# Kernel tuning notes

Hardware: AMD Instinct MI355X
Metric: run time of the kernel (lower is better)

## Reference

```python
import jax, jax.numpy as jnp
import numpy as np

SCALE = 10000.0
EPS = 1e-5


def _extract_patches(x):
    # x: [B,28,28] int32 -> [B,28,28,9] (3x3 neighborhoods, zero-padded)
    xp = jnp.pad(x, ((0, 0), (1, 1), (1, 1)))
    ps = [xp[:, i:i + 28, j:j + 28] for i in range(3) for j in range(3)]
    return jnp.stack(ps, axis=-1)


def _bn_eval(x, g, b, m, v):
    inv = g / jnp.sqrt(v + EPS)
    return x * inv[None, :, None, None] + (b - m * inv)[None, :, None, None]


def _maxpool2(x):
    return jax.lax.reduce_window(x, -jnp.inf, jax.lax.max,
                                 (1, 1, 2, 2), (1, 1, 2, 2), 'VALID')


def _conv(x, w, b):
    y = jax.lax.conv_general_dilated(x, w, (1, 1), 'SAME',
                                     dimension_numbers=('NCHW', 'OIHW', 'NCHW'))
    return y + b[None, :, None, None]


def setup_inputs() -> dict:
    key = jax.random.key(0)
    ks = jax.random.split(key, 24)
    B = 1024
    inp = {}
    inp['x_img'] = jax.random.randint(ks[0], (B, 28, 28), 0, 256, dtype=jnp.int32)
    # quantized conv1 weights: round(w * 10000), signed
    inp['y_int'] = jax.random.randint(ks[1], (16, 9), 0, 20001, dtype=jnp.int32) - 10000
    inp['bias1'] = jax.random.normal(ks[2], (16,), jnp.float32)
    for i, (c, kg, kb, km, kv) in enumerate([(16, 3, 4, 5, 6), (32, 7, 8, 9, 10), (64, 11, 12, 13, 14)]):
        j = i + 1
        inp[f'g{j}'] = jax.random.uniform(ks[kg], (c,), jnp.float32, 0.5, 1.5)
        inp[f'b{j}'] = jax.random.normal(ks[kb], (c,), jnp.float32)
        inp[f'm{j}'] = jax.random.normal(ks[km], (c,), jnp.float32)
        inp[f'v{j}'] = jax.random.uniform(ks[kv], (c,), jnp.float32, 0.5, 1.5)
    inp['w2'] = jax.random.normal(ks[15], (32, 16, 3, 3), jnp.float32) * 0.1
    inp['bias2'] = jax.random.normal(ks[16], (32,), jnp.float32)
    inp['w3'] = jax.random.normal(ks[17], (64, 32, 3, 3), jnp.float32) * 0.1
    inp['bias3'] = jax.random.normal(ks[18], (64,), jnp.float32)
    inp['w_fc1'] = jax.random.normal(ks[19], (128, 576), jnp.float32) * 0.05
    inp['b_fc1'] = jax.random.normal(ks[20], (128,), jnp.float32)
    inp['w_fc2'] = jax.random.normal(ks[21], (10, 128), jnp.float32) * 0.1
    inp['b_fc2'] = jax.random.normal(ks[22], (10,), jnp.float32)
    return inp


def reference(x_img, y_int, bias1, g1, b1, m1, v1, w2, bias2, g2, b2, m2, v2,
              w3, bias3, g3, b3, m3, v3, w_fc1, b_fc1, w_fc2, b_fc2):
    # IPFE first conv: exact integer inner product <patch, y>, then /10000 + bias
    patches = _extract_patches(x_img)                      # [B,28,28,9] int32
    ip = jnp.einsum('bhwk,ok->bohw', patches, y_int)       # exact int32 dot
    feat = ip.astype(jnp.float32) / SCALE + bias1[None, :, None, None]  # [B,16,28,28]
    feat = _maxpool2(jax.nn.relu(_bn_eval(feat, g1, b1, m1, v1)))       # [B,16,14,14]
    feat = _maxpool2(jax.nn.relu(_bn_eval(_conv(feat, w2, bias2), g2, b2, m2, v2)))  # [B,32,7,7]
    feat = _maxpool2(jax.nn.relu(_bn_eval(_conv(feat, w3, bias3), g3, b3, m3, v3)))  # [B,64,3,3]
    flat = feat.reshape(feat.shape[0], -1)                 # [B,576]
    h = jax.nn.relu(flat @ w_fc1.T + b_fc1)                # [B,128] (dropout: eval mode)
    return h @ w_fc2.T + b_fc2                             # [B,10]
```

## Files before the change

kernel.cpp:

```cpp
#include <hip/hip_runtime.h>
#include <hip/hip_bf16.h>

#define EPS 1e-5f

typedef __attribute__((ext_vector_type(8))) short bf16x8;
typedef __attribute__((ext_vector_type(4))) float f32x4;
typedef unsigned short ushort_t;
#define MFMA16(a, b, c) __builtin_amdgcn_mfma_f32_16x16x32_bf16(a, b, c, 0, 0, 0)

#define CST_OFF  144
#define W2F_H    1024
#define W3F_H    6144
#define WFC1F_H  24576
#define PREP_ITEMS (368 + 5120 + 18432 + 81920)

__device__ __forceinline__ unsigned short f2bf(float f) {
    unsigned int u = __builtin_bit_cast(unsigned int, f);
    return (unsigned short)((u + 0x7fffu + ((u >> 16) & 1u)) >> 16);
}

__global__ __launch_bounds__(256) void prep_kernel(
    const int* __restrict__ y_int,
    const float* __restrict__ w2, const float* __restrict__ w3,
    const float* __restrict__ wfc1,
    const float* __restrict__ bias1,
    const float* __restrict__ g1, const float* __restrict__ b1,
    const float* __restrict__ m1, const float* __restrict__ v1,
    const float* __restrict__ g2, const float* __restrict__ b2,
    const float* __restrict__ m2, const float* __restrict__ v2,
    const float* __restrict__ bias2,
    const float* __restrict__ g3, const float* __restrict__ b3,
    const float* __restrict__ m3, const float* __restrict__ v3,
    const float* __restrict__ bias3,
    float* __restrict__ ws)
{
    unsigned short* wsh = (unsigned short*)ws;
    int i = blockIdx.x * 256 + threadIdx.x;
    if (i < 144) {
        int k = i >> 4, c = i & 15;
        ws[i] = (float)y_int[c * 9 + k];
    } else if (i < 368) {
        int idx = i - 144;
        if (idx < 16) { int c = idx;
            ws[CST_OFF + idx] = g1[c] * rsqrtf(v1[c] + EPS) * 1e-4f;
        } else if (idx < 32) { int c = idx - 16;
            float inv = g1[c] * rsqrtf(v1[c] + EPS);
            ws[CST_OFF + idx] = bias1[c] * inv + b1[c] - m1[c] * inv;
        } else if (idx < 64) { int c = idx - 32;
            ws[CST_OFF + idx] = g2[c] * rsqrtf(v2[c] + EPS);
        } else if (idx < 96) { int c = idx - 64;
            float inv = g2[c] * rsqrtf(v2[c] + EPS);
            ws[CST_OFF + idx] = bias2[c] * inv + b2[c] - m2[c] * inv;
        } else if (idx < 160) { int c = idx - 96;
            ws[CST_OFF + idx] = g3[c] * rsqrtf(v3[c] + EPS);
        } else { int c = idx - 160;
            float inv = g3[c] * rsqrtf(v3[c] + EPS);
            ws[CST_OFF + idx] = bias3[c] * inv + b3[c] - m3[c] * inv;
        }
    } else {
        int e = i - 368;
        if (e < 5120) {
            int m = e / 2560, r = e % 2560, s = r >> 9, l = (r >> 3) & 63, j = e & 7;
            int kl  = ((l >> 4) << 3) + j;
            int tap = 2 * s + (kl >> 4), ci = kl & 15;
            int ch  = m * 16 + (l & 15);
            float v = (tap < 9) ? w2[ch * 144 + ci * 9 + tap] : 0.f;
            wsh[W2F_H + e] = f2bf(v);
        } else if (e < 5120 + 18432) {
            int e3 = e - 5120;
            int mt = e3 / 4608, r = e3 % 4608, ks = r >> 9, l = (r >> 3) & 63, j = e3 & 7;
            int ch = mt * 16 + (l & 15), ci = ((l >> 4) << 3) + j;
            wsh[W3F_H + e3] = f2bf(w3[ch * 288 + ci * 9 + ks]);
        } else {
            int ef = e - 23552;
            int mt = ef / 10240, r = ef % 10240;
            int ks = r >> 9, l = (r >> 3) & 63, j = ef & 7;
            int ch = mt * 16 + (l & 15);
            int kp = ks * 32 + ((l >> 4) << 3) + j;
            int w  = kp / 160, lk = kp - w * 160;
            float v = 0.f;
            if (lk < 144) v = wfc1[ch * 576 + (w * 16 + lk / 9) * 9 + (lk % 9)];
            wsh[WFC1F_H + ef] = f2bf(v);
        }
    }
}

__global__ __launch_bounds__(256, 4) void fused_cnn(
    const int* __restrict__ x_img,
    const float* __restrict__ ws,
    const float* __restrict__ bfc1,
    const float* __restrict__ wfc2, const float* __restrict__ bfc2,
    float* __restrict__ out)
{
    const int tid  = threadIdx.x;
    const int lane = tid & 63;
    const int wv   = __builtin_amdgcn_readfirstlane(tid >> 6);
    const int img  = blockIdx.x;
    const unsigned short* wsh = (const unsigned short*)ws;

    __shared__ __align__(16) char s_f1[8192];
    __shared__ __align__(16) char s_f2[5184];
    ushort_t* FLAT = (ushort_t*)s_f1;
    float*    Hp   = (float*)(s_f1 + 1536);

    {
        uint4 z = make_uint4(0u, 0u, 0u, 0u);
        if (tid < 120) {
            int c0 = tid / 60, b = tid % 60, pos;
            if (b < 16)      pos = b;
            else if (b < 32) pos = 240 + (b - 16);
            else if (b < 46) pos = (b - 31) * 16;
            else             pos = (b - 45) * 16 + 15;
            *(uint4*)(s_f1 + c0 * 4096 + pos * 16) = z;
        } else if (tid < 248) {
            int zz = tid - 120;
            int q = zz / 32, b = zz % 32, pos;
            if (b < 9)       pos = b;
            else if (b < 18) pos = 72 + (b - 9);
            else if (b < 25) pos = (b - 17) * 9;
            else             pos = (b - 24) * 9 + 8;
            *(uint4*)(s_f2 + q * 1296 + pos * 16) = z;
        }
    }

    if (tid < 196) {
        int ph = tid / 14, pw = tid - (tid / 14) * 14;
        const int* xp = x_img + img * 784;
        int ry0 = 2 * ph - 1, cx0 = 2 * pw - 1;
        float px[4][4];
        #pragma unroll
        for (int dy = 0; dy < 4; dy++) {
            int ry = ry0 + dy;
            int ryc = min(max(ry, 0), 27);
            bool rok = (unsigned)ry < 28u;
            #pragma unroll
            for (int dx = 0; dx < 4; dx++) {
                int cx = cx0 + dx;
                int cxc = min(max(cx, 0), 27);
                float v = (float)xp[ryc * 28 + cxc];
                px[dy][dx] = (rok && (unsigned)cx < 28u) ? v : 0.f;
            }
        }
        float acc[16][4];
        #pragma unroll
        for (int c = 0; c < 16; c++) {
            acc[c][0] = 0.f; acc[c][1] = 0.f; acc[c][2] = 0.f; acc[c][3] = 0.f;
        }
        #pragma unroll
        for (int k = 0; k < 9; k++) {
            int ty = k / 3, tx = k % 3;
            float x0 = px[ty][tx],     x1 = px[ty][tx + 1];
            float x2 = px[ty + 1][tx], x3 = px[ty + 1][tx + 1];
            const float4* yw = (const float4*)(ws + k * 16);
            float4 wA = yw[0], wB = yw[1], wC = yw[2], wD = yw[3];
            float wr[16] = {wA.x, wA.y, wA.z, wA.w, wB.x, wB.y, wB.z, wB.w,
                            wC.x, wC.y, wC.z, wC.w, wD.x, wD.y, wD.z, wD.w};
            #pragma unroll
            for (int c = 0; c < 16; c++) {
                float w = wr[c];
                acc[c][0] += w * x0; acc[c][1] += w * x1;
                acc[c][2] += w * x2; acc[c][3] += w * x3;
            }
        }
        unsigned int pk[8];
        #pragma unroll
        for (int c = 0; c < 16; c += 2) {
            float mx0 = fmaxf(fmaxf(acc[c][0], acc[c][1]), fmaxf(acc[c][2], acc[c][3]));
            float r0  = fmaxf(mx0 * ws[CST_OFF + c] + ws[CST_OFF + 16 + c], 0.f);
            float mx1 = fmaxf(fmaxf(acc[c+1][0], acc[c+1][1]), fmaxf(acc[c+1][2], acc[c+1][3]));
            float r1  = fmaxf(mx1 * ws[CST_OFF + c + 1] + ws[CST_OFF + 16 + c + 1], 0.f);
            pk[c >> 1] = (unsigned int)f2bf(r0) | ((unsigned int)f2bf(r1) << 16);
        }
        int pos = (ph + 1) * 16 + (pw + 1);
        *(uint4*)(s_f1 + pos * 16)        = make_uint4(pk[0], pk[1], pk[2], pk[3]);
        *(uint4*)(s_f1 + 4096 + pos * 16) = make_uint4(pk[4], pk[5], pk[6], pk[7]);
    }
    __syncthreads();

    {
        const int x = lane & 15, g = lane >> 4;
        const int t2 = g >> 1, c0 = g & 1;
        bf16x8 A2[2][5];
        #pragma unroll
        for (int m = 0; m < 2; m++)
            #pragma unroll
            for (int s = 0; s < 5; s++)
                A2[m][s] = *(const bf16x8*)(const void*)(wsh + W2F_H + ((m * 5 + s) * 64 + lane) * 8);
        int voff[5];
        #pragma unroll
        for (int s = 0; s < 5; s++) {
            int tap = 2 * s + t2;
            int dy = (tap < 9) ? tap / 3 : 0, dx = (tap < 9) ? tap % 3 : 0;
            voff[s] = c0 * 4096 + (dy * 16 + x + dx) * 16;
        }
        float a2v[2][4], c2v[2][4];
        #pragma unroll
        for (int m = 0; m < 2; m++)
            #pragma unroll
            for (int r = 0; r < 4; r++) {
                int ch = m * 16 + g * 4 + r;
                a2v[m][r] = ws[CST_OFF + 32 + ch];
                c2v[m][r] = ws[CST_OFF + 64 + ch];
            }
        for (int p = wv; p < 7; p += 4) {
            const char* bp = s_f1 + p * 512;
            bf16x8 B0[5], B1[5];
            #pragma unroll
            for (int s = 0; s < 5; s++) {
                B0[s] = *(const bf16x8*)(const void*)(bp + voff[s]);
                B1[s] = *(const bf16x8*)(const void*)(bp + 256 + voff[s]);
            }
            #pragma unroll
            for (int m = 0; m < 2; m++) {
                f32x4 a0 = {0.f, 0.f, 0.f, 0.f}, a1 = {0.f, 0.f, 0.f, 0.f};
                #pragma unroll
                for (int s = 0; s < 5; s++) {
                    a0 = MFMA16(A2[m][s], B0[s], a0);
                    a1 = MFMA16(A2[m][s], B1[s], a1);
                }
                float hp[4];
                #pragma unroll
                for (int r = 0; r < 4; r++) {
                    float vp = fmaxf(a0[r], a1[r]);
                    hp[r] = fmaxf(vp, __shfl_xor(vp, 1));
                }
                if (!(x & 1) && x < 14) {
                    int xp2 = x >> 1;
                    int pp  = (p + 1) * 9 + xp2 + 1;
                    int ch0 = m * 16 + g * 4;
                    unsigned int lo = (unsigned int)f2bf(fmaxf(hp[0] * a2v[m][0] + c2v[m][0], 0.f)) |
                                      ((unsigned int)f2bf(fmaxf(hp[1] * a2v[m][1] + c2v[m][1], 0.f)) << 16);
                    unsigned int hi = (unsigned int)f2bf(fmaxf(hp[2] * a2v[m][2] + c2v[m][2], 0.f)) |
                                      ((unsigned int)f2bf(fmaxf(hp[3] * a2v[m][3] + c2v[m][3], 0.f)) << 16);
                    *(uint2*)(s_f2 + (ch0 >> 3) * 1296 + pp * 16 + (ch0 & 7) * 2) = make_uint2(lo, hi);
                }
            }
        }
    }
    __syncthreads();

    {
        const int mt = wv;
        bf16x8 A3[9];
        #pragma unroll
        for (int ks = 0; ks < 9; ks++)
            A3[ks] = *(const bf16x8*)(const void*)(wsh + W3F_H + ((mt * 9 + ks) * 64 + lane) * 8);
        const int x8 = lane & 7, ry = (lane >> 3) & 1, qg = lane >> 4;
        int voff3[9];
        #pragma unroll
        for (int ks = 0; ks < 9; ks++) {
            int dy = ks / 3, dx = ks % 3;
            voff3[ks] = qg * 1296 + ((ry + dy) * 9 + x8 + dx) * 16;
        }
        float a3v[4], c3v[4];
        #pragma unroll
        for (int r = 0; r < 4; r++) {
            int ch = mt * 16 + qg * 4 + r;
            a3v[r] = ws[CST_OFF + 96 + ch];
            c3v[r] = ws[CST_OFF + 160 + ch];
        }
        if (lane < 16) FLAT[wv * 160 + 144 + lane] = 0;
        #pragma unroll
        for (int t = 0; t < 3; t++) {
            bf16x8 bb[9];
            #pragma unroll
            for (int ks = 0; ks < 9; ks++)
                bb[ks] = *(const bf16x8*)(const void*)(s_f2 + t * 288 + voff3[ks]);
            f32x4 acc = {0.f, 0.f, 0.f, 0.f};
            #pragma unroll
            for (int ks = 0; ks < 9; ks++)
                acc = MFMA16(A3[ks], bb[ks], acc);
            float hp[4];
            #pragma unroll
            for (int r = 0; r < 4; r++) {
                float vp = fmaxf(acc[r], __shfl_xor(acc[r], 8));
                hp[r] = fmaxf(vp, __shfl_xor(vp, 1));
            }
            if (ry == 0 && !(x8 & 1) && x8 < 6) {
                int xp3 = x8 >> 1;
                #pragma unroll
                for (int r = 0; r < 4; r++) {
                    float v = fmaxf(hp[r] * a3v[r] + c3v[r], 0.f);
                    FLAT[wv * 160 + (qg * 4 + r) * 9 + t * 3 + xp3] = f2bf(v);
                }
            }
        }

        const int g = lane >> 4;
        bf16x8 BV[5];
        #pragma unroll
        for (int ksl = 0; ksl < 5; ksl++)
            BV[ksl] = *(const bf16x8*)(const void*)(FLAT + (wv * 5 + ksl) * 32 + g * 8);
        #pragma unroll
        for (int mtf = 0; mtf < 8; mtf++) {
            f32x4 acc = {0.f, 0.f, 0.f, 0.f};
            #pragma unroll
            for (int ksl = 0; ksl < 5; ksl++) {
                int ks = wv * 5 + ksl;
                bf16x8 a = *(const bf16x8*)(const void*)(wsh + WFC1F_H + ((mtf * 20 + ks) * 64 + lane) * 8);
                acc = MFMA16(a, BV[ksl], acc);
            }
            if ((lane & 15) == 0) {
                int ch0 = mtf * 16 + g * 4;
                #pragma unroll
                for (int r = 0; r < 4; r++)
                    Hp[wv * 128 + ch0 + r] = acc[r];
            }
        }
    }
    __syncthreads();

    if (tid < 160) {
        int o = tid / 16, l = tid & 15;
        float a = 0.f;
        #pragma unroll
        for (int k = l; k < 128; k += 16) {
            float h = Hp[k] + Hp[128 + k] + Hp[256 + k] + Hp[384 + k] + bfc1[k];
            h = fmaxf(h, 0.f);
            a += h * wfc2[o * 128 + k];
        }
        a += __shfl_xor(a, 8);
        a += __shfl_xor(a, 4);
        a += __shfl_xor(a, 2);
        a += __shfl_xor(a, 1);
        if (l == 0) out[img * 10 + o] = a + bfc2[o];
    }
}

extern "C" void kernel_launch(void* const* d_in, const int* in_sizes, int n_in,
                              void* d_out, int out_size, void* d_ws, size_t ws_size,
                              hipStream_t stream) {
    float* ws = (float*)d_ws;
    prep_kernel<<<(PREP_ITEMS + 255) / 256, 256, 0, stream>>>(
        (const int*)d_in[1],
        (const float*)d_in[15],
        (const float*)d_in[17],
        (const float*)d_in[19],
        (const float*)d_in[2],
        (const float*)d_in[3], (const float*)d_in[4], (const float*)d_in[5], (const float*)d_in[6],
        (const float*)d_in[7], (const float*)d_in[8], (const float*)d_in[9], (const float*)d_in[10],
        (const float*)d_in[16],
        (const float*)d_in[11], (const float*)d_in[12], (const float*)d_in[13], (const float*)d_in[14],
        (const float*)d_in[18],
        ws);
    fused_cnn<<<1024, 256, 0, stream>>>(
        (const int*)d_in[0],
        ws,
        (const float*)d_in[20],
        (const float*)d_in[21], (const float*)d_in[22],
        (float*)d_out);
}
```

Before: 27.22 us.

## Fuse weight prep into main kernel and process two images per block

Removes the separate prep kernel. Each block now computes the BN constants and conv1 weights into shared memory and converts the w2, w3 and fc1 weights to bf16 fragments directly from global fp32. Blocks grow to 512 threads and handle two images. The fc1 stage is restructured so each wave owns 16 output channels across both images, with ReLU and bias folded in. This drops one launch and the workspace round trip, but every block now repeats the strided fp32 weight loads and bf16 conversions, and an extra barrier is added.

```diff
diff --git a/kernel.cpp b/kernel.cpp
--- a/kernel.cpp
+++ b/kernel.cpp
@@ -8,188 +8,171 @@
 typedef unsigned short ushort_t;
 #define MFMA16(a, b, c) __builtin_amdgcn_mfma_f32_16x16x32_bf16(a, b, c, 0, 0, 0)
 
-#define CST_OFF  144
-#define W2F_H    1024
-#define W3F_H    6144
-#define WFC1F_H  24576
-#define PREP_ITEMS (368 + 5120 + 18432 + 81920)
-
 __device__ __forceinline__ unsigned short f2bf(float f) {
     unsigned int u = __builtin_bit_cast(unsigned int, f);
     return (unsigned short)((u + 0x7fffu + ((u >> 16) & 1u)) >> 16);
 }
 
-__global__ __launch_bounds__(256) void prep_kernel(
-    const int* __restrict__ y_int,
-    const float* __restrict__ w2, const float* __restrict__ w3,
-    const float* __restrict__ wfc1,
+__global__ __launch_bounds__(512, 2) void fused_cnn(
+    const int* __restrict__ x_img, const int* __restrict__ y_int,
     const float* __restrict__ bias1,
     const float* __restrict__ g1, const float* __restrict__ b1,
     const float* __restrict__ m1, const float* __restrict__ v1,
     const float* __restrict__ g2, const float* __restrict__ b2,
     const float* __restrict__ m2, const float* __restrict__ v2,
-    const float* __restrict__ bias2,
     const float* __restrict__ g3, const float* __restrict__ b3,
     const float* __restrict__ m3, const float* __restrict__ v3,
-    const float* __restrict__ bias3,
-    float* __restrict__ ws)
-{
-    unsigned short* wsh = (unsigned short*)ws;
-    int i = blockIdx.x * 256 + threadIdx.x;
-    if (i < 144) {
-        int k = i >> 4, c = i & 15;
-        ws[i] = (float)y_int[c * 9 + k];
-    } else if (i < 368) {
-        int idx = i - 144;
-        if (idx < 16) { int c = idx;
-            ws[CST_OFF + idx] = g1[c] * rsqrtf(v1[c] + EPS) * 1e-4f;
-        } else if (idx < 32) { int c = idx - 16;
-            float inv = g1[c] * rsqrtf(v1[c] + EPS);
-            ws[CST_OFF + idx] = bias1[c] * inv + b1[c] - m1[c] * inv;
-        } else if (idx < 64) { int c = idx - 32;
-            ws[CST_OFF + idx] = g2[c] * rsqrtf(v2[c] + EPS);
-        } else if (idx < 96) { int c = idx - 64;
-            float inv = g2[c] * rsqrtf(v2[c] + EPS);
-            ws[CST_OFF + idx] = bias2[c] * inv + b2[c] - m2[c] * inv;
-        } else if (idx < 160) { int c = idx - 96;
-            ws[CST_OFF + idx] = g3[c] * rsqrtf(v3[c] + EPS);
-        } else { int c = idx - 160;
-            float inv = g3[c] * rsqrtf(v3[c] + EPS);
-            ws[CST_OFF + idx] = bias3[c] * inv + b3[c] - m3[c] * inv;
-        }
-    } else {
-        int e = i - 368;
-        if (e < 5120) {
-            int m = e / 2560, r = e % 2560, s = r >> 9, l = (r >> 3) & 63, j = e & 7;
-            int kl  = ((l >> 4) << 3) + j;
-            int tap = 2 * s + (kl >> 4), ci = kl & 15;
-            int ch  = m * 16 + (l & 15);
-            float v = (tap < 9) ? w2[ch * 144 + ci * 9 + tap] : 0.f;
-            wsh[W2F_H + e] = f2bf(v);
-        } else if (e < 5120 + 18432) {
-            int e3 = e - 5120;
-            int mt = e3 / 4608, r = e3 % 4608, ks = r >> 9, l = (r >> 3) & 63, j = e3 & 7;
-            int ch = mt * 16 + (l & 15), ci = ((l >> 4) << 3) + j;
-            wsh[W3F_H + e3] = f2bf(w3[ch * 288 + ci * 9 + ks]);
-        } else {
-            int ef = e - 23552;
-            int mt = ef / 10240, r = ef % 10240;
-            int ks = r >> 9, l = (r >> 3) & 63, j = ef & 7;
-            int ch = mt * 16 + (l & 15);
-            int kp = ks * 32 + ((l >> 4) << 3) + j;
-            int w  = kp / 160, lk = kp - w * 160;
-            float v = 0.f;
-            if (lk < 144) v = wfc1[ch * 576 + (w * 16 + lk / 9) * 9 + (lk % 9)];
-            wsh[WFC1F_H + ef] = f2bf(v);
-        }
-    }
-}
-
-__global__ __launch_bounds__(256, 4) void fused_cnn(
-    const int* __restrict__ x_img,
-    const float* __restrict__ ws,
-    const float* __restrict__ bfc1,
+    const float* __restrict__ w2, const float* __restrict__ bias2,
+    const float* __restrict__ w3, const float* __restrict__ bias3,
+    const float* __restrict__ wfc1, const float* __restrict__ bfc1,
     const float* __restrict__ wfc2, const float* __restrict__ bfc2,
     float* __restrict__ out)
 {
     const int tid  = threadIdx.x;
     const int lane = tid & 63;
     const int wv   = __builtin_amdgcn_readfirstlane(tid >> 6);
-    const int img  = blockIdx.x;
-    const unsigned short* wsh = (const unsigned short*)ws;
-
-    __shared__ __align__(16) char s_f1[8192];
-    __shared__ __align__(16) char s_f2[5184];
-    ushort_t* FLAT = (ushort_t*)s_f1;
-    float*    Hp   = (float*)(s_f1 + 1536);
-
+    const int ig   = wv >> 2;
+    const int wv4  = wv & 3;
+
+    __shared__ __align__(16) char  s_f1[2][8192];
+    __shared__ __align__(16) char  s_f2[2][5184];
+    __shared__ __align__(16) float s_cst[224];
+    __shared__ __align__(16) float s_yt[144];
+    float* H = (float*)(&s_f1[0][0] + 2048);
+
+    if (tid < 224) {
+        int idx = tid;
+        float v;
+        if (idx < 16) { int c = idx;
+            v = g1[c] * rsqrtf(v1[c] + EPS) * 1e-4f;
+        } else if (idx < 32) { int c = idx - 16;
+            float inv = g1[c] * rsqrtf(v1[c] + EPS);
+            v = bias1[c] * inv + b1[c] - m1[c] * inv;
+        } else if (idx < 64) { int c = idx - 32;
+            v = g2[c] * rsqrtf(v2[c] + EPS);
+        } else if (idx < 96) { int c = idx - 64;
+            float inv = g2[c] * rsqrtf(v2[c] + EPS);
+            v = bias2[c] * inv + b2[c] - m2[c] * inv;
+        } else if (idx < 160) { int c = idx - 96;
+            v = g3[c] * rsqrtf(v3[c] + EPS);
+        } else { int c = idx - 160;
+            float inv = g3[c] * rsqrtf(v3[c] + EPS);
+            v = bias3[c] * inv + b3[c] - m3[c] * inv;
+        }
+        s_cst[idx] = v;
+    } else if (tid < 368) {
+        int t2 = tid - 224;
+        int k = t2 >> 4, c = t2 & 15;
+        s_yt[t2] = (float)y_int[c * 9 + k];
+    }
     {
         uint4 z = make_uint4(0u, 0u, 0u, 0u);
-        if (tid < 120) {
-            int c0 = tid / 60, b = tid % 60, pos;
-            if (b < 16)      pos = b;
-            else if (b < 32) pos = 240 + (b - 16);
-            else if (b < 46) pos = (b - 31) * 16;
-            else             pos = (b - 45) * 16 + 15;
-            *(uint4*)(s_f1 + c0 * 4096 + pos * 16) = z;
-        } else if (tid < 248) {
-            int zz = tid - 120;
-            int q = zz / 32, b = zz % 32, pos;
-            if (b < 9)       pos = b;
-            else if (b < 18) pos = 72 + (b - 9);
-            else if (b < 25) pos = (b - 17) * 9;
-            else             pos = (b - 24) * 9 + 8;
-            *(uint4*)(s_f2 + q * 1296 + pos * 16) = z;
-        }
-    }
-
-    if (tid < 196) {
-        int ph = tid / 14, pw = tid - (tid / 14) * 14;
-        const int* xp = x_img + img * 784;
-        int ry0 = 2 * ph - 1, cx0 = 2 * pw - 1;
-        float px[4][4];
-        #pragma unroll
-        for (int dy = 0; dy < 4; dy++) {
-            int ry = ry0 + dy;
-            int ryc = min(max(ry, 0), 27);
-            bool rok = (unsigned)ry < 28u;
-            #pragma unroll
-            for (int dx = 0; dx < 4; dx++) {
-                int cx = cx0 + dx;
-                int cxc = min(max(cx, 0), 27);
-                float v = (float)xp[ryc * 28 + cxc];
-                px[dy][dx] = (rok && (unsigned)cx < 28u) ? v : 0.f;
-            }
-        }
-        float acc[16][4];
-        #pragma unroll
-        for (int c = 0; c < 16; c++) {
-            acc[c][0] = 0.f; acc[c][1] = 0.f; acc[c][2] = 0.f; acc[c][3] = 0.f;
-        }
-        #pragma unroll
-        for (int k = 0; k < 9; k++) {
-            int ty = k / 3, tx = k % 3;
-            float x0 = px[ty][tx],     x1 = px[ty][tx + 1];
-            float x2 = px[ty + 1][tx], x3 = px[ty + 1][tx + 1];
-            const float4* yw = (const float4*)(ws + k * 16);
-            float4 wA = yw[0], wB = yw[1], wC = yw[2], wD = yw[3];
-            float wr[16] = {wA.x, wA.y, wA.z, wA.w, wB.x, wB.y, wB.z, wB.w,
-                            wC.x, wC.y, wC.z, wC.w, wD.x, wD.y, wD.z, wD.w};
+        if (tid < 496) {
+            int zi = tid / 248, zz = tid % 248;
+            if (zz < 120) {
+                int c0 = zz / 60, b = zz % 60, pos;
+                if (b < 16)      pos = b;
+                else if (b < 32) pos = 240 + (b - 16);
+                else if (b < 46) pos = (b - 31) * 16;
+                else             pos = (b - 45) * 16 + 15;
+                *(uint4*)(&s_f1[zi][0] + c0 * 4096 + pos * 16) = z;
+            } else {
+                int zz2 = zz - 120;
+                int q = zz2 / 32, b = zz2 % 32, pos;
+                if (b < 9)       pos = b;
+                else if (b < 18) pos = 72 + (b - 9);
+                else if (b < 25) pos = (b - 17) * 9;
+                else             pos = (b - 24) * 9 + 8;
+                *(uint4*)(&s_f2[zi][0] + q * 1296 + pos * 16) = z;
+            }
+        }
+    }
+    __syncthreads();
+
+    {
+        const int t = tid & 255;
+        const int g1i = tid >> 8;
+        if (t < 196) {
+            int ph = t / 14, pw = t - (t / 14) * 14;
+            const int* xp = x_img + (blockIdx.x * 2 + g1i) * 784;
+            int ry0 = 2 * ph - 1, cx0 = 2 * pw - 1;
+            float px[4][4];
+            #pragma unroll
+            for (int dy = 0; dy < 4; dy++) {
+                int ry = ry0 + dy;
+                int ryc = min(max(ry, 0), 27);
+                bool rok = (unsigned)ry < 28u;
+                #pragma unroll
+                for (int dx = 0; dx < 4; dx++) {
+                    int cx = cx0 + dx;
+                    int cxc = min(max(cx, 0), 27);
+                    float v = (float)xp[ryc * 28 + cxc];
+                    px[dy][dx] = (rok && (unsigned)cx < 28u) ? v : 0.f;
+                }
+            }
+            float acc[16][4];
             #pragma unroll
             for (int c = 0; c < 16; c++) {
-                float w = wr[c];
-                acc[c][0] += w * x0; acc[c][1] += w * x1;
-                acc[c][2] += w * x2; acc[c][3] += w * x3;
-            }
-        }
-        unsigned int pk[8];
-        #pragma unroll
-        for (int c = 0; c < 16; c += 2) {
-            float mx0 = fmaxf(fmaxf(acc[c][0], acc[c][1]), fmaxf(acc[c][2], acc[c][3]));
-            float r0  = fmaxf(mx0 * ws[CST_OFF + c] + ws[CST_OFF + 16 + c], 0.f);
-            float mx1 = fmaxf(fmaxf(acc[c+1][0], acc[c+1][1]), fmaxf(acc[c+1][2], acc[c+1][3]));
-            float r1  = fmaxf(mx1 * ws[CST_OFF + c + 1] + ws[CST_OFF + 16 + c + 1], 0.f);
-            pk[c >> 1] = (unsigned int)f2bf(r0) | ((unsigned int)f2bf(r1) << 16);
-        }
-        int pos = (ph + 1) * 16 + (pw + 1);
-        *(uint4*)(s_f1 + pos * 16)        = make_uint4(pk[0], pk[1], pk[2], pk[3]);
-        *(uint4*)(s_f1 + 4096 + pos * 16) = make_uint4(pk[4], pk[5], pk[6], pk[7]);
+                acc[c][0] = 0.f; acc[c][1] = 0.f; acc[c][2] = 0.f; acc[c][3] = 0.f;
+            }
+            #pragma unroll
+            for (int k = 0; k < 9; k++) {
+                int ty = k / 3, tx = k % 3;
+                float x0 = px[ty][tx],     x1 = px[ty][tx + 1];
+                float x2 = px[ty + 1][tx], x3 = px[ty + 1][tx + 1];
+                const float4* yw = (const float4*)(&s_yt[k * 16]);
+                float4 wA = yw[0], wB = yw[1], wC = yw[2], wD = yw[3];
+                float wr[16] = {wA.x, wA.y, wA.z, wA.w, wB.x, wB.y, wB.z, wB.w,
+                                wC.x, wC.y, wC.z, wC.w, wD.x, wD.y, wD.z, wD.w};
+                #pragma unroll
+                for (int c = 0; c < 16; c++) {
+                    float w = wr[c];
+                    acc[c][0] += w * x0; acc[c][1] += w * x1;
+                    acc[c][2] += w * x2; acc[c][3] += w * x3;
+                }
+            }
+            unsigned int pk[8];
+            #pragma unroll
+            for (int c = 0; c < 16; c += 2) {
+                float mx0 = fmaxf(fmaxf(acc[c][0], acc[c][1]), fmaxf(acc[c][2], acc[c][3]));
+                float r0  = fmaxf(mx0 * s_cst[c] + s_cst[16 + c], 0.f);
+                float mx1 = fmaxf(fmaxf(acc[c+1][0], acc[c+1][1]), fmaxf(acc[c+1][2], acc[c+1][3]));
+                float r1  = fmaxf(mx1 * s_cst[c + 1] + s_cst[16 + c + 1], 0.f);
+                pk[c >> 1] = (unsigned int)f2bf(r0) | ((unsigned int)f2bf(r1) << 16);
+            }
+            int pos = (ph + 1) * 16 + (pw + 1);
+            *(uint4*)(&s_f1[g1i][0] + pos * 16)        = make_uint4(pk[0], pk[1], pk[2], pk[3]);
+            *(uint4*)(&s_f1[g1i][0] + 4096 + pos * 16) = make_uint4(pk[4], pk[5], pk[6], pk[7]);
+        }
     }
     __syncthreads();
 
     {
         const int x = lane & 15, g = lane >> 4;
-        const int t2 = g >> 1, c0 = g & 1;
+        const int tapb = g >> 1, c0 = g & 1;
         bf16x8 A2[2][5];
         #pragma unroll
-        for (int m = 0; m < 2; m++)
-            #pragma unroll
-            for (int s = 0; s < 5; s++)
-                A2[m][s] = *(const bf16x8*)(const void*)(wsh + W2F_H + ((m * 5 + s) * 64 + lane) * 8);
+        for (int m = 0; m < 2; m++) {
+            const float* wrow = w2 + (m * 16 + x) * 144;
+            #pragma unroll
+            for (int s = 0; s < 5; s++) {
+                int tap = 2 * s + tapb;
+                bf16x8 fr;
+                if (tap < 9) {
+                    const float* wp = wrow + c0 * 72 + tap;
+                    #pragma unroll
+                    for (int j = 0; j < 8; j++) fr[j] = (short)f2bf(wp[j * 9]);
+                } else {
+                    #pragma unroll
+                    for (int j = 0; j < 8; j++) fr[j] = 0;
+                }
+                A2[m][s] = fr;
+            }
+        }
         int voff[5];
         #pragma unroll
         for (int s = 0; s < 5; s++) {
-            int tap = 2 * s + t2;
+            int tap = 2 * s + tapb;
             int dy = (tap < 9) ? tap / 3 : 0, dx = (tap < 9) ? tap % 3 : 0;
             voff[s] = c0 * 4096 + (dy * 16 + x + dx) * 16;
         }
@@ -199,11 +182,11 @@
             #pragma unroll
             for (int r = 0; r < 4; r++) {
                 int ch = m * 16 + g * 4 + r;
-                a2v[m][r] = ws[CST_OFF + 32 + ch];
-                c2v[m][r] = ws[CST_OFF + 64 + ch];
-            }
-        for (int p = wv; p < 7; p += 4) {
-            const char* bp = s_f1 + p * 512;
+                a2v[m][r] = s_cst[32 + ch];
+                c2v[m][r] = s_cst[64 + ch];
+            }
+        for (int p = wv4; p < 7; p += 4) {
+            const char* bp = &s_f1[ig][0] + p * 512;
             bf16x8 B0[5], B1[5];
             #pragma unroll
             for (int s = 0; s < 5; s++) {
@@ -232,20 +215,25 @@
                                       ((unsigned int)f2bf(fmaxf(hp[1] * a2v[m][1] + c2v[m][1], 0.f)) << 16);
                     unsigned int hi = (unsigned int)f2bf(fmaxf(hp[2] * a2v[m][2] + c2v[m][2], 0.f)) |
                                       ((unsigned int)f2bf(fmaxf(hp[3] * a2v[m][3] + c2v[m][3], 0.f)) << 16);
-                    *(uint2*)(s_f2 + (ch0 >> 3) * 1296 + pp * 16 + (ch0 & 7) * 2) = make_uint2(lo, hi);
-                }
-            }
-        }
-    }
-    __syncthreads();
-
-    {
-        const int mt = wv;
+                    *(uint2*)(&s_f2[ig][0] + (ch0 >> 3) * 1296 + pp * 16 + (ch0 & 7) * 2) = make_uint2(lo, hi);
+                }
+            }
+        }
+    }
+    __syncthreads();
+
+    {
+        const int mt = wv4;
+        const float* w3r = w3 + (mt * 16 + (lane & 15)) * 288;
+        const int x8 = lane & 7, ry = (lane >> 3) & 1, qg = lane >> 4;
         bf16x8 A3[9];
         #pragma unroll
-        for (int ks = 0; ks < 9; ks++)
-            A3[ks] = *(const bf16x8*)(const void*)(wsh + W3F_H + ((mt * 9 + ks) * 64 + lane) * 8);
-        const int x8 = lane & 7, ry = (lane >> 3) & 1, qg = lane >> 4;
+        for (int ks = 0; ks < 9; ks++) {
+            bf16x8 fr;
+            #pragma unroll
+            for (int j = 0; j < 8; j++) fr[j] = (short)f2bf(w3r[(qg * 8 + j) * 9 + ks]);
+            A3[ks] = fr;
+        }
         int voff3[9];
         #pragma unroll
         for (int ks = 0; ks < 9; ks++) {
@@ -256,16 +244,16 @@
         #pragma unroll
         for (int r = 0; r < 4; r++) {
             int ch = mt * 16 + qg * 4 + r;
-            a3v[r] = ws[CST_OFF + 96 + ch];
-            c3v[r] = ws[CST_OFF + 160 + ch];
-        }
-        if (lane < 16) FLAT[wv * 160 + 144 + lane] = 0;
+            a3v[r] = s_cst[96 + ch];
+            c3v[r] = s_cst[160 + ch];
+        }
+        ushort_t* FLAT = (ushort_t*)&s_f1[ig][0];
         #pragma unroll
         for (int t = 0; t < 3; t++) {
             bf16x8 bb[9];
             #pragma unroll
             for (int ks = 0; ks < 9; ks++)
-                bb[ks] = *(const bf16x8*)(const void*)(s_f2 + t * 288 + voff3[ks]);
+                bb[ks] = *(const bf16x8*)(const void*)(&s_f2[ig][0] + t * 288 + voff3[ks]);
             f32x4 acc = {0.f, 0.f, 0.f, 0.f};
             #pragma unroll
             for (int ks = 0; ks < 9; ks++)
@@ -278,75 +266,71 @@
             }
             if (ry == 0 && !(x8 & 1) && x8 < 6) {
                 int xp3 = x8 >> 1;
+                int ch0 = mt * 16 + qg * 4;
                 #pragma unroll
                 for (int r = 0; r < 4; r++) {
                     float v = fmaxf(hp[r] * a3v[r] + c3v[r], 0.f);
-                    FLAT[wv * 160 + (qg * 4 + r) * 9 + t * 3 + xp3] = f2bf(v);
-                }
-            }
-        }
-
+                    FLAT[(ch0 + r) * 9 + t * 3 + xp3] = f2bf(v);
+                }
+            }
+        }
+    }
+    __syncthreads();
+
+    {
         const int g = lane >> 4;
-        bf16x8 BV[5];
-        #pragma unroll
-        for (int ksl = 0; ksl < 5; ksl++)
-            BV[ksl] = *(const bf16x8*)(const void*)(FLAT + (wv * 5 + ksl) * 32 + g * 8);
-        #pragma unroll
-        for (int mtf = 0; mtf < 8; mtf++) {
-            f32x4 acc = {0.f, 0.f, 0.f, 0.f};
-            #pragma unroll
-            for (int ksl = 0; ksl < 5; ksl++) {
-                int ks = wv * 5 + ksl;
-                bf16x8 a = *(const bf16x8*)(const void*)(wsh + WFC1F_H + ((mtf * 20 + ks) * 64 + lane) * 8);
-                acc = MFMA16(a, BV[ksl], acc);
-            }
-            if ((lane & 15) == 0) {
-                int ch0 = mtf * 16 + g * 4;
-                #pragma unroll
-                for (int r = 0; r < 4; r++)
-                    Hp[wv * 128 + ch0 + r] = acc[r];
-            }
-        }
-    }
-    __syncthreads();
-
-    if (tid < 160) {
-        int o = tid / 16, l = tid & 15;
+        const int ib = (lane >> 3) & 1;
+        const float* wf = wfc1 + (wv * 16 + (lane & 15)) * 576;
+        const ushort_t* FLATi = (const ushort_t*)&s_f1[ib][0];
+        f32x4 acc = {0.f, 0.f, 0.f, 0.f};
+        #pragma unroll
+        for (int ks = 0; ks < 18; ks++) {
+            int k0 = ks * 32 + g * 8;
+            float4 fa = *(const float4*)(wf + k0);
+            float4 fb = *(const float4*)(wf + k0 + 4);
+            bf16x8 a;
+            a[0] = (short)f2bf(fa.x); a[1] = (short)f2bf(fa.y);
+            a[2] = (short)f2bf(fa.z); a[3] = (short)f2bf(fa.w);
+            a[4] = (short)f2bf(fb.x); a[5] = (short)f2bf(fb.y);
+            a[6] = (short)f2bf(fb.z); a[7] = (short)f2bf(fb.w);
+            bf16x8 bv = *(const bf16x8*)(const void*)(FLATi + ks * 32 + g * 8);
+            acc = MFMA16(a, bv, acc);
+        }
+        if ((lane & 7) == 0) {
+            int ch0 = wv * 16 + g * 4;
+            #pragma unroll
+            for (int r = 0; r < 4; r++)
+                H[ib * 128 + ch0 + r] = fmaxf(acc[r] + bfc1[ch0 + r], 0.f);
+        }
+    }
+    __syncthreads();
+
+    if (tid < 320) {
+        int im = tid / 160, t = tid - im * 160;
+        int o = t / 16, l = t & 15;
         float a = 0.f;
         #pragma unroll
-        for (int k = l; k < 128; k += 16) {
-            float h = Hp[k] + Hp[128 + k] + Hp[256 + k] + Hp[384 + k] + bfc1[k];
-            h = fmaxf(h, 0.f);
-            a += h * wfc2[o * 128 + k];
-        }
+        for (int k = l; k < 128; k += 16)
+            a += H[im * 128 + k] * wfc2[o * 128 + k];
         a += __shfl_xor(a, 8);
         a += __shfl_xor(a, 4);
         a += __shfl_xor(a, 2);
         a += __shfl_xor(a, 1);
-        if (l == 0) out[img * 10 + o] = a + bfc2[o];
+        if (l == 0) out[(blockIdx.x * 2 + im) * 10 + o] = a + bfc2[o];
     }
 }
 
 extern "C" void kernel_launch(void* const* d_in, const int* in_sizes, int n_in,
                               void* d_out, int out_size, void* d_ws, size_t ws_size,
                               hipStream_t stream) {
-    float* ws = (float*)d_ws;
-    prep_kernel<<<(PREP_ITEMS + 255) / 256, 256, 0, stream>>>(
-        (const int*)d_in[1],
-        (const float*)d_in[15],
-        (const float*)d_in[17],
-        (const float*)d_in[19],
-        (const float*)d_in[2],
+    fused_cnn<<<512, 512, 0, stream>>>(
+        (const int*)d_in[0],   (const int*)d_in[1],   (const float*)d_in[2],
         (const float*)d_in[3], (const float*)d_in[4], (const float*)d_in[5], (const float*)d_in[6],
         (const float*)d_in[7], (const float*)d_in[8], (const float*)d_in[9], (const float*)d_in[10],
-        (const float*)d_in[16],
-        (const float*)d_in[11], (const float*)d_in[12], (const float*)d_in[13], (const float*)d_in[14],
-        (const float*)d_in[18],
-        ws);
-    fused_cnn<<<1024, 256, 0, stream>>>(
-        (const int*)d_in[0],
-        ws,
-        (const float*)d_in[20],
-        (const float*)d_in[21], (const float*)d_in[22],
+        (const float*)d_in[11],(const float*)d_in[12],(const float*)d_in[13],(const float*)d_in[14],
+        (const float*)d_in[15],(const float*)d_in[16],
+        (const float*)d_in[17],(const float*)d_in[18],
+        (const float*)d_in[19],(const float*)d_in[20],
+        (const float*)d_in[21],(const float*)d_in[22],
         (float*)d_out);
 }
```

After: 68.33 us. 151% more time.

## Compute conv1 with bf16 MFMA using split-precision weights and staged pixels

Applied to the files above, without the earlier changes.

Replaces the scalar FMA conv1 (each of 196 threads computing 16 channels over a 4x4 pixel window) with MFMA 16x16x32 bf16. The input image is first staged into padded LDS as duplicated bf16 pixels, and the integer weights are split into hi and lo bf16 parts so the products stay exact. Maxpool is done with a shuffle and the BN/ReLU result is written to s_f1. This adds an extra barrier and LDS staging, and relies on the pixel values (0-255) being exactly representable in bf16.

```diff
diff --git a/kernel.cpp b/kernel.cpp
--- a/kernel.cpp
+++ b/kernel.cpp
@@ -5,6 +5,7 @@
 
 typedef __attribute__((ext_vector_type(8))) short bf16x8;
 typedef __attribute__((ext_vector_type(4))) float f32x4;
+typedef __attribute__((ext_vector_type(4))) unsigned int u32x4;
 typedef unsigned short ushort_t;
 #define MFMA16(a, b, c) __builtin_amdgcn_mfma_f32_16x16x32_bf16(a, b, c, 0, 0, 0)
 
@@ -12,7 +13,8 @@
 #define W2F_H    1024
 #define W3F_H    6144
 #define WFC1F_H  24576
-#define PREP_ITEMS (368 + 5120 + 18432 + 81920)
+#define W1F_H    106496
+#define PREP_ITEMS (368 + 5120 + 18432 + 81920 + 1024)
 
 __device__ __forceinline__ unsigned short f2bf(float f) {
     unsigned int u = __builtin_bit_cast(unsigned int, f);
@@ -71,7 +73,7 @@
             int mt = e3 / 4608, r = e3 % 4608, ks = r >> 9, l = (r >> 3) & 63, j = e3 & 7;
             int ch = mt * 16 + (l & 15), ci = ((l >> 4) << 3) + j;
             wsh[W3F_H + e3] = f2bf(w3[ch * 288 + ci * 9 + ks]);
-        } else {
+        } else if (e < 23552 + 81920) {
             int ef = e - 23552;
             int mt = ef / 10240, r = ef % 10240;
             int ks = r >> 9, l = (r >> 3) & 63, j = ef & 7;
@@ -81,6 +83,20 @@
             float v = 0.f;
             if (lk < 144) v = wfc1[ch * 576 + (w * 16 + lk / 9) * 9 + (lk % 9)];
             wsh[WFC1F_H + ef] = f2bf(v);
+        } else {
+            int e4 = e - 105472;
+            int half = e4 >> 9, l = (e4 >> 3) & 63, j = e4 & 7;
+            int g = l >> 4, ch = l & 15;
+            float w = 0.f;
+            if (g < 3 && !(j & 1) && (j >> 1) < 3)
+                w = (float)y_int[ch * 9 + g * 3 + (j >> 1)];
+            unsigned short hib = f2bf(w);
+            if (half == 0) {
+                wsh[W1F_H + e4] = hib;
+            } else {
+                float hif = __builtin_bit_cast(float, (unsigned int)hib << 16);
+                wsh[W1F_H + e4] = f2bf(w - hif);
+            }
         }
     }
 }
@@ -98,88 +114,104 @@
     const int img  = blockIdx.x;
     const unsigned short* wsh = (const unsigned short*)ws;
 
-    __shared__ __align__(16) char s_f1[8192];
-    __shared__ __align__(16) char s_f2[5184];
+    __shared__ __align__(16) char         s_f1[8192];
+    __shared__ __align__(16) char         s_f2[5184];
+    __shared__ __align__(16) unsigned int s_px[1200];
     ushort_t* FLAT = (ushort_t*)s_f1;
     float*    Hp   = (float*)(s_f1 + 1536);
 
+    const int* xp = x_img + img * 784;
+    for (int i = tid; i < 784; i += 256) {
+        int r = i / 28, c = i - r * 28;
+        float f = (float)xp[i];
+        unsigned int b = __builtin_bit_cast(unsigned int, f) >> 16;
+        s_px[(r + 1) * 40 + c + 1] = b | (b << 16);
+    }
     {
         uint4 z = make_uint4(0u, 0u, 0u, 0u);
-        if (tid < 120) {
-            int c0 = tid / 60, b = tid % 60, pos;
+        if (tid < 28) {
+            unsigned int* row = s_px + (tid + 1) * 40;
+            row[0] = 0u;
+            #pragma unroll
+            for (int c = 29; c < 40; c++) row[c] = 0u;
+        } else if (tid < 48) {
+            int j = tid - 28;
+            int row = (j < 10) ? 0 : 29, ch = (j < 10) ? j : j - 10;
+            *(uint4*)((char*)s_px + row * 160 + ch * 16) = z;
+        } else if (tid < 168) {
+            int zz = tid - 48;
+            int c0 = zz / 60, b = zz % 60, pos;
             if (b < 16)      pos = b;
             else if (b < 32) pos = 240 + (b - 16);
             else if (b < 46) pos = (b - 31) * 16;
             else             pos = (b - 45) * 16 + 15;
             *(uint4*)(s_f1 + c0 * 4096 + pos * 16) = z;
-        } else if (tid < 248) {
-            int zz = tid - 120;
-            int q = zz / 32, b = zz % 32, pos;
-            if (b < 9)       pos = b;
-            else if (b < 18) pos = 72 + (b - 9);
-            else if (b < 25) pos = (b - 17) * 9;
-            else             pos = (b - 24) * 9 + 8;
-            *(uint4*)(s_f2 + q * 1296 + pos * 16) = z;
-        }
-    }
-
-    if (tid < 196) {
-        int ph = tid / 14, pw = tid - (tid / 14) * 14;
-        const int* xp = x_img + img * 784;
-        int ry0 = 2 * ph - 1, cx0 = 2 * pw - 1;
-        float px[4][4];
-        #pragma unroll
-        for (int dy = 0; dy < 4; dy++) {
-            int ry = ry0 + dy;
-            int ryc = min(max(ry, 0), 27);
-            bool rok = (unsigned)ry < 28u;
-            #pragma unroll
-            for (int dx = 0; dx < 4; dx++) {
-                int cx = cx0 + dx;
-                int cxc = min(max(cx, 0), 27);
-                float v = (float)xp[ryc * 28 + cxc];
-                px[dy][dx] = (rok && (unsigned)cx < 28u) ? v : 0.f;
-            }
-        }
-        float acc[16][4];
-        #pragma unroll
-        for (int c = 0; c < 16; c++) {
-            acc[c][0] = 0.f; acc[c][1] = 0.f; acc[c][2] = 0.f; acc[c][3] = 0.f;
-        }
-        #pragma unroll
-        for (int k = 0; k < 9; k++) {
-            int ty = k / 3, tx = k % 3;
-            float x0 = px[ty][tx],     x1 = px[ty][tx + 1];
-            float x2 = px[ty + 1][tx], x3 = px[ty + 1][tx + 1];
-            const float4* yw = (const float4*)(ws + k * 16);
-            float4 wA = yw[0], wB = yw[1], wC = yw[2], wD = yw[3];
-            float wr[16] = {wA.x, wA.y, wA.z, wA.w, wB.x, wB.y, wB.z, wB.w,
-                            wC.x, wC.y, wC.z, wC.w, wD.x, wD.y, wD.z, wD.w};
-            #pragma unroll
-            for (int c = 0; c < 16; c++) {
-                float w = wr[c];
-                acc[c][0] += w * x0; acc[c][1] += w * x1;
-                acc[c][2] += w * x2; acc[c][3] += w * x3;
-            }
-        }
-        unsigned int pk[8];
-        #pragma unroll
-        for (int c = 0; c < 16; c += 2) {
-            float mx0 = fmaxf(fmaxf(acc[c][0], acc[c][1]), fmaxf(acc[c][2], acc[c][3]));
-            float r0  = fmaxf(mx0 * ws[CST_OFF + c] + ws[CST_OFF + 16 + c], 0.f);
-            float mx1 = fmaxf(fmaxf(acc[c+1][0], acc[c+1][1]), fmaxf(acc[c+1][2], acc[c+1][3]));
-            float r1  = fmaxf(mx1 * ws[CST_OFF + c + 1] + ws[CST_OFF + 16 + c + 1], 0.f);
-            pk[c >> 1] = (unsigned int)f2bf(r0) | ((unsigned int)f2bf(r1) << 16);
-        }
-        int pos = (ph + 1) * 16 + (pw + 1);
-        *(uint4*)(s_f1 + pos * 16)        = make_uint4(pk[0], pk[1], pk[2], pk[3]);
-        *(uint4*)(s_f1 + 4096 + pos * 16) = make_uint4(pk[4], pk[5], pk[6], pk[7]);
+        } else {
+            int i0 = tid - 168;
+            #pragma unroll
+            for (int rep = 0; rep < 2; rep++) {
+                int i2 = i0 + rep * 88;
+                if (i2 < 128) {
+                    int q = i2 >> 5, b = i2 & 31, pos;
+                    if (b < 9)       pos = b;
+                    else if (b < 18) pos = 72 + (b - 9);
+                    else if (b < 25) pos = (b - 17) * 9;
+                    else             pos = (b - 24) * 9 + 8;
+                    *(uint4*)(s_f2 + q * 1296 + pos * 16) = z;
+                }
+            }
+        }
+    }
+    __syncthreads();
+
+    {
+        bf16x8 A1H = *(const bf16x8*)(const void*)(wsh + W1F_H + lane * 8);
+        bf16x8 A1L = *(const bf16x8*)(const void*)(wsh + W1F_H + (64 + lane) * 8);
+        const int n = lane & 15, g = lane >> 4;
+        const int gp = (g < 2) ? g : 2;
+        float a1v[4], c1v[4];
+        #pragma unroll
+        for (int r = 0; r < 4; r++) {
+            int ch = g * 4 + r;
+            a1v[r] = ws[CST_OFF + ch];
+            c1v[r] = ws[CST_OFF + 16 + ch];
+        }
+        for (int p1 = wv; p1 < 14; p1 += 4) {
+            const unsigned int* rb = s_px + (2 * p1 + gp) * 40 + n;
+            #pragma unroll
+            for (int xt = 0; xt < 2; xt++) {
+                const unsigned int* r0 = rb + xt * 16;
+                u32x4 t0 = {r0[0], r0[1], r0[2], r0[3]};
+                u32x4 t1 = {r0[40], r0[41], r0[42], r0[43]};
+                bf16x8 B0 = __builtin_bit_cast(bf16x8, t0);
+                bf16x8 B1 = __builtin_bit_cast(bf16x8, t1);
+                f32x4 aA = {0.f, 0.f, 0.f, 0.f}, aB = {0.f, 0.f, 0.f, 0.f};
+                aA = MFMA16(A1L, B0, aA); aA = MFMA16(A1H, B0, aA);
+                aB = MFMA16(A1L, B1, aB); aB = MFMA16(A1H, B1, aB);
+                float hp[4];
+                #pragma unroll
+                for (int r = 0; r < 4; r++) {
+                    float vp = fmaxf(aA[r], aB[r]);
+                    hp[r] = fmaxf(vp, __shfl_xor(vp, 1));
+                }
+                if (!(n & 1) && (xt == 0 || n < 12)) {
+                    int xpo = xt * 8 + (n >> 1);
+                    int pos = (p1 + 1) * 16 + (xpo + 1);
+                    int ch0 = g * 4;
+                    unsigned int lo = (unsigned int)f2bf(fmaxf(hp[0] * a1v[0] + c1v[0], 0.f)) |
+                                      ((unsigned int)f2bf(fmaxf(hp[1] * a1v[1] + c1v[1], 0.f)) << 16);
+                    unsigned int hi = (unsigned int)f2bf(fmaxf(hp[2] * a1v[2] + c1v[2], 0.f)) |
+                                      ((unsigned int)f2bf(fmaxf(hp[3] * a1v[3] + c1v[3], 0.f)) << 16);
+                    *(uint2*)(s_f1 + (ch0 >> 3) * 4096 + pos * 16 + (ch0 & 7) * 2) = make_uint2(lo, hi);
+                }
+            }
+        }
     }
     __syncthreads();
 
     {
         const int x = lane & 15, g = lane >> 4;
-        const int t2 = g >> 1, c0 = g & 1;
+        const int tapb = g >> 1, c0 = g & 1;
         bf16x8 A2[2][5];
         #pragma unroll
         for (int m = 0; m < 2; m++)
@@ -189,7 +221,7 @@
         int voff[5];
         #pragma unroll
         for (int s = 0; s < 5; s++) {
-            int tap = 2 * s + t2;
+            int tap = 2 * s + tapb;
             int dy = (tap < 9) ? tap / 3 : 0, dx = (tap < 9) ? tap % 3 : 0;
             voff[s] = c0 * 4096 + (dy * 16 + x + dx) * 16;
         }
```

Result: faster. 26.55 us (median of 2 runs) (-2.5%).
